# Performance work log

Hardware: AMD Instinct MI355X
Metric: run time of the kernel (lower is better)

## Reference

```python
import jax, jax.numpy as jnp
import numpy as np

B, N, NC, C = 8, 16384, 64, 256

def setup_inputs() -> dict:
    key = jax.random.key(0)
    k1, k2, k3, k4, k5, k6 = jax.random.split(key, 6)
    s = 1.0 / np.sqrt(C)
    return {
        "point_features": jax.random.normal(k1, (B, N, C), dtype=jnp.float32),
        "centroid_features": jax.random.normal(k2, (B, NC, C), dtype=jnp.float32),
        "W_p": jax.random.uniform(k3, (C, C), jnp.float32, -s, s),   # point_transform weight (in,out)
        "b_p": jax.random.uniform(k4, (C,), jnp.float32, -s, s),
        "W_c": jax.random.uniform(k5, (C, C), jnp.float32, -s, s),   # centroid_transform weight (in,out)
        "b_c": jax.random.uniform(k6, (C,), jnp.float32, -s, s),
    }

def reference(point_features, centroid_features, W_p, b_p, W_c, b_c):
    # Linear projections
    p_proj = jnp.einsum('bnc,cd->bnd', point_features, W_p) + b_p      # (B,N,C)
    c_proj = jnp.einsum('bkc,cd->bkd', centroid_features, W_c) + b_c   # (B,NC,C)
    # Unscaled cross-attention scores and softmax over centroids
    scores = jnp.einsum('bnd,bkd->bnk', p_proj, c_proj)                # (B,N,NC)
    weights = jax.nn.softmax(scores, axis=-1)
    # Weighted sum of RAW centroid features (values not projected)
    weighted = jnp.einsum('bnk,bkc->bnc', weights, centroid_features)  # (B,N,C)
    return point_features + weighted
```

## Files before the change

kernel.cpp:

```cpp
#include <hip/hip_runtime.h>

#define B_  8
#define N_  16384
#define NC_ 64
#define C_  256

typedef __attribute__((ext_vector_type(8))) short bf16x8;
typedef __attribute__((ext_vector_type(4))) float f32x4;

#define WS_GT   0
#define WS_BLOB 262144
#define WS_S0   786432
#define WS_WFB  788480
#define WS_H    789504
#define WS_BB   790528

__device__ __forceinline__ unsigned rne_bf16(float f) {
    unsigned u = __float_as_uint(f);
    return (u + 0x7fffu + ((u >> 16) & 1u)) >> 16;
}
__device__ __forceinline__ float bf2f(short s) {
    return __uint_as_float(((unsigned)(unsigned short)s) << 16);
}
__device__ __forceinline__ f32x4 mfma16(bf16x8 a, bf16x8 b, f32x4 c) {
    return __builtin_amdgcn_mfma_f32_16x16x32_bf16(a, b, c, 0, 0, 0);
}

__global__ __launch_bounds__(256) void k_p1(const float* __restrict__ Wp,
        const float* __restrict__ Wc, const float* __restrict__ bc,
        const float* __restrict__ bp, float* __restrict__ ws) {
    __shared__ float WpL[256];
    __shared__ float bpL[256];
    __shared__ float red[4];
    int c = blockIdx.x, t = threadIdx.x;
    WpL[t] = Wp[(size_t)c*C_ + t];
    bpL[t] = bp[t];
    float bcv = bc[t];
    __syncthreads();

    const float* wcr = Wc + (size_t)t*C_;
    float acc = 0.f;
    #pragma unroll 8
    for (int d = 0; d < C_; d += 4) {
        f32x4 wv = *(const f32x4*)(wcr + d);
        f32x4 wp = *(const f32x4*)(WpL + d);
        acc += wv[0]*wp[0] + wv[1]*wp[1] + wv[2]*wp[2] + wv[3]*wp[3];
    }
    ws[WS_GT/4 + c*C_ + t] = acc;

    float hp = bcv * WpL[t];
    #pragma unroll
    for (int m = 32; m; m >>= 1) hp += __shfl_xor(hp, m);
    if ((t & 63) == 0) red[t >> 6] = hp;
    __syncthreads();
    if (t == 0) ws[WS_H/4 + c] = red[0] + red[1] + red[2] + red[3];

    if (c == 0) {
        float aw = 0.f;
        #pragma unroll 8
        for (int d = 0; d < C_; d += 4) {
            f32x4 wv = *(const f32x4*)(wcr + d);
            f32x4 b4 = *(const f32x4*)(bpL + d);
            aw += wv[0]*b4[0] + wv[1]*b4[1] + wv[2]*b4[2] + wv[3]*b4[3];
        }
        ws[WS_WFB/4 + t] = aw;
        float pb = bcv * bpL[t];
        #pragma unroll
        for (int m = 32; m; m >>= 1) pb += __shfl_xor(pb, m);
        __syncthreads();
        if ((t & 63) == 0) red[t >> 6] = pb;
        __syncthreads();
        if (t == 0) ws[WS_BB/4] = red[0] + red[1] + red[2] + red[3];
    }
}

__global__ __launch_bounds__(256) void k_p2(const float* __restrict__ Cf,
        float* __restrict__ ws) {
    __shared__ float CfL[8][256];
    __shared__ float wfbL[256];
    int b = blockIdx.x >> 3, kg = blockIdx.x & 7;
    int t = threadIdx.x;
    const float* cfb = Cf + ((size_t)b*NC_ + kg*8)*C_;
    #pragma unroll
    for (int kk = 0; kk < 8; ++kk) CfL[kk][t] = cfb[kk*C_ + t];
    wfbL[t] = ws[WS_WFB/4 + t];
    float hv = ws[WS_H/4 + t];
    float bb = ws[WS_BB/4];
    __syncthreads();

    char* vtB  = (char*)ws + WS_BLOB + (size_t)b*65536;
    char* cftB = vtB + 32768;

    {
        int nf  = ((t >> 5) << 1) | ((t >> 2) & 1);
        int rho = ((t >> 3) & 3) * 4 + (t & 3);
        unsigned base = (unsigned)(nf*2048 + rho*128);
        #pragma unroll
        for (int kk = 0; kk < 8; ++kk) {
            *(unsigned short*)(cftB + base + (kg*8 + kk)*2) =
                (unsigned short)rne_bf16(CfL[kk][t]);
        }
    }

    float acc[8];
    #pragma unroll
    for (int kk = 0; kk < 8; ++kk) acc[kk] = hv;
    const float* gtr = ws + WS_GT/4 + (size_t)t*C_;
    #pragma unroll 4
    for (int e = 0; e < C_; e += 4) {
        f32x4 g4 = *(const f32x4*)(gtr + e);
        #pragma unroll
        for (int kk = 0; kk < 8; ++kk) {
            f32x4 c4 = *(const f32x4*)(&CfL[kk][e]);
            acc[kk] += g4[0]*c4[0] + g4[1]*c4[1] + g4[2]*c4[2] + g4[3]*c4[3];
        }
    }
    #pragma unroll
    for (int kk = 0; kk < 8; ++kk) {
        int row = kg*8 + kk;
        *(unsigned short*)(vtB + row*512 + t*2) = (unsigned short)rne_bf16(acc[kk]);
    }

    int w = t >> 6, l = t & 63;
    #pragma unroll
    for (int kk = 2*w; kk < 2*w + 2; ++kk) {
        float s = 0.f;
        #pragma unroll
        for (int j = 0; j < 4; ++j) s += CfL[kk][l + 64*j] * wfbL[l + 64*j];
        #pragma unroll
        for (int m = 32; m; m >>= 1) s += __shfl_xor(s, m);
        if (l == 0) ws[WS_S0/4 + b*NC_ + kg*8 + kk] = s + bb;
    }
}

__global__ __launch_bounds__(256, 4) void k_main(const float* __restrict__ P,
        const char* __restrict__ blob, const float* __restrict__ s0g,
        float* __restrict__ out) {
    __shared__ __align__(16) char wbAll[8192];

    int b    = blockIdx.x >> 8;
    int tile = blockIdx.x & 255;
    int tid = threadIdx.x;
    int w   = tid >> 6;
    int l   = tid & 63;
    int l15 = l & 15;
    int g   = l >> 4;

    const char* blobV = blob + (size_t)b*65536;
    const char* blobC = blobV + 32768;

    int prow = tile*64 + w*16 + l15;
    const float* Prow = P + ((size_t)b*N_ + prow)*C_;

    f32x4 sacc[4];
    #pragma unroll
    for (int mf = 0; mf < 4; ++mf)
        sacc[mf] = *(const f32x4*)(s0g + b*NC_ + mf*16 + g*4);

    bf16x8 phi[8], plo[8];
    f32x4 pA0 = *(const f32x4*)(Prow + g*8);
    f32x4 pA1 = *(const f32x4*)(Prow + g*8 + 4);
    f32x4 pB0 = *(const f32x4*)(Prow + g*8 + 32);
    f32x4 pB1 = *(const f32x4*)(Prow + g*8 + 36);

    #pragma unroll
    for (int kk = 0; kk < 8; ++kk) {
        bf16x8 vh0 = *(const bf16x8*)(blobV + (0*16 + l15)*512 + kk*64 + g*16);
        bf16x8 vh1 = *(const bf16x8*)(blobV + (1*16 + l15)*512 + kk*64 + g*16);
        bf16x8 vh2 = *(const bf16x8*)(blobV + (2*16 + l15)*512 + kk*64 + g*16);
        bf16x8 vh3 = *(const bf16x8*)(blobV + (3*16 + l15)*512 + kk*64 + g*16);
        #pragma unroll
        for (int h = 0; h < 2; ++h) {
            f32x4 src = h ? pA1 : pA0;
            #pragma unroll
            for (int j = 0; j < 4; ++j) {
                float f  = src[j];
                unsigned hb = rne_bf16(f);
                float hf = __uint_as_float(hb << 16);
                unsigned lb = rne_bf16(f - hf);
                phi[kk][h*4 + j] = (short)hb;
                plo[kk][h*4 + j] = (short)lb;
            }
        }
        pA0 = pB0; pA1 = pB1;
        if (kk < 6) {
            pB0 = *(const f32x4*)(Prow + g*8 + (kk+2)*32);
            pB1 = *(const f32x4*)(Prow + g*8 + (kk+2)*32 + 4);
        }
        sacc[0] = mfma16(vh0, phi[kk], sacc[0]);
        sacc[1] = mfma16(vh1, phi[kk], sacc[1]);
        sacc[2] = mfma16(vh2, phi[kk], sacc[2]);
        sacc[3] = mfma16(vh3, phi[kk], sacc[3]);
        sacc[0] = mfma16(vh0, plo[kk], sacc[0]);
        sacc[1] = mfma16(vh1, plo[kk], sacc[1]);
        sacc[2] = mfma16(vh2, plo[kk], sacc[2]);
        sacc[3] = mfma16(vh3, plo[kk], sacc[3]);
    }

    float mx = -3.0e38f;
    #pragma unroll
    for (int mf = 0; mf < 4; ++mf)
        #pragma unroll
        for (int r = 0; r < 4; ++r) mx = fmaxf(mx, sacc[mf][r]);
    mx = fmaxf(mx, __shfl_xor(mx, 16));
    mx = fmaxf(mx, __shfl_xor(mx, 32));
    float sum = 0.f;
    #pragma unroll
    for (int mf = 0; mf < 4; ++mf)
        #pragma unroll
        for (int r = 0; r < 4; ++r) {
            float e = __expf(sacc[mf][r] - mx);
            sacc[mf][r] = e; sum += e;
        }
    sum += __shfl_xor(sum, 16);
    sum += __shfl_xor(sum, 32);
    float inv = 1.0f / sum;

    char* wb = wbAll + w*2048;
    #pragma unroll
    for (int mf = 0; mf < 4; ++mf) {
        unsigned w01 = rne_bf16(sacc[mf][0]*inv) | (rne_bf16(sacc[mf][1]*inv) << 16);
        unsigned w23 = rne_bf16(sacc[mf][2]*inv) | (rne_bf16(sacc[mf][3]*inv) << 16);
        unsigned off = ((unsigned)(l15*128 + mf*32 + g*8)) ^ ((unsigned)(l15 & 7) << 4);
        uint2 v; v.x = w01; v.y = w23;
        *(uint2*)(wb + off) = v;
    }
    unsigned woff0 = ((unsigned)(l15*128 +  0 + g*16)) ^ ((unsigned)(l15 & 7) << 4);
    unsigned woff1 = ((unsigned)(l15*128 + 64 + g*16)) ^ ((unsigned)(l15 & 7) << 4);
    bf16x8 wf0 = *(const bf16x8*)(wb + woff0);
    bf16x8 wf1 = *(const bf16x8*)(wb + woff1);

    size_t rowbase = ((size_t)b*N_ + prow) * C_;
    #pragma unroll
    for (int nf = 0; nf < 16; ++nf) {
        const char* cbase = blobC + nf*2048 + l15*128 + g*16;
        bf16x8 cf0 = *(const bf16x8*)(cbase);
        bf16x8 cf1 = *(const bf16x8*)(cbase + 64);
        f32x4 o = {0.f, 0.f, 0.f, 0.f};
        o = mfma16(cf0, wf0, o);
        o = mfma16(cf1, wf1, o);
        int kf = nf >> 1, e0 = (nf & 1) * 4;
        f32x4 res;
        #pragma unroll
        for (int r = 0; r < 4; ++r)
            res[r] = bf2f(phi[kf][e0 + r]) + bf2f(plo[kf][e0 + r]) + o[r];
        *(f32x4*)(out + rowbase + (nf >> 1)*32 + (nf & 1)*4 + g*8) = res;
    }
}

extern "C" void kernel_launch(void* const* d_in, const int* in_sizes, int n_in,
                              void* d_out, int out_size, void* d_ws, size_t ws_size,
                              hipStream_t stream) {
    const float* P  = (const float*)d_in[0];
    const float* Cf = (const float*)d_in[1];
    const float* Wp = (const float*)d_in[2];
    const float* bp = (const float*)d_in[3];
    const float* Wc = (const float*)d_in[4];
    const float* bc = (const float*)d_in[5];
    float* out = (float*)d_out;
    float* ws  = (float*)d_ws;

    k_p1<<<256, 256, 0, stream>>>(Wp, Wc, bc, bp, ws);
    k_p2<<<64, 256, 0, stream>>>(Cf, ws);
    k_main<<<B_*(N_/64), 256, 0, stream>>>(P, (const char*)d_ws + WS_BLOB,
                                           ws + WS_S0/4, out);
}
```

Measured before the change: 354.7 us.

## Reload exact point features for residual and use natural centroid layout in output pass

The main kernel now issues all sixteen point-feature vector loads up front instead of a two-deep rolling prefetch. It drops the per-element bf16 hi/lo arrays kept alive across the softmax. The residual add now rereads the fp32 point features from global memory (likely L2-resident), using a simple contiguous column layout per output fragment. The centroid-value blob is written in a plain row-major transposed layout to match. This lowers register pressure and makes the residual exact, at the cost of a second read of the point rows and non-contiguous 16-byte output stores.

```diff
diff --git a/kernel.cpp b/kernel.cpp
--- a/kernel.cpp
+++ b/kernel.cpp
@@ -18,9 +18,6 @@
 __device__ __forceinline__ unsigned rne_bf16(float f) {
     unsigned u = __float_as_uint(f);
     return (u + 0x7fffu + ((u >> 16) & 1u)) >> 16;
-}
-__device__ __forceinline__ float bf2f(short s) {
-    return __uint_as_float(((unsigned)(unsigned short)s) << 16);
 }
 __device__ __forceinline__ f32x4 mfma16(bf16x8 a, bf16x8 b, f32x4 c) {
     return __builtin_amdgcn_mfma_f32_16x16x32_bf16(a, b, c, 0, 0, 0);
@@ -91,15 +88,10 @@
     char* vtB  = (char*)ws + WS_BLOB + (size_t)b*65536;
     char* cftB = vtB + 32768;
 
-    {
-        int nf  = ((t >> 5) << 1) | ((t >> 2) & 1);
-        int rho = ((t >> 3) & 3) * 4 + (t & 3);
-        unsigned base = (unsigned)(nf*2048 + rho*128);
-        #pragma unroll
-        for (int kk = 0; kk < 8; ++kk) {
-            *(unsigned short*)(cftB + base + (kg*8 + kk)*2) =
-                (unsigned short)rne_bf16(CfL[kk][t]);
-        }
+    #pragma unroll
+    for (int kk = 0; kk < 8; ++kk) {
+        *(unsigned short*)(cftB + t*128 + (kg*8 + kk)*2) =
+            (unsigned short)rne_bf16(CfL[kk][t]);
     }
 
     float acc[8];
@@ -150,18 +142,19 @@
     const char* blobC = blobV + 32768;
 
     int prow = tile*64 + w*16 + l15;
-    const float* Prow = P + ((size_t)b*N_ + prow)*C_;
-
+    size_t rowbase = ((size_t)b*N_ + prow) * C_;
+    const float* Prow = P + rowbase + g*8;
+
+    f32x4 pf[16];
+    #pragma unroll
+    for (int kk = 0; kk < 8; ++kk) {
+        pf[2*kk]   = *(const f32x4*)(Prow + kk*32);
+        pf[2*kk+1] = *(const f32x4*)(Prow + kk*32 + 4);
+    }
     f32x4 sacc[4];
     #pragma unroll
     for (int mf = 0; mf < 4; ++mf)
         sacc[mf] = *(const f32x4*)(s0g + b*NC_ + mf*16 + g*4);
-
-    bf16x8 phi[8], plo[8];
-    f32x4 pA0 = *(const f32x4*)(Prow + g*8);
-    f32x4 pA1 = *(const f32x4*)(Prow + g*8 + 4);
-    f32x4 pB0 = *(const f32x4*)(Prow + g*8 + 32);
-    f32x4 pB1 = *(const f32x4*)(Prow + g*8 + 36);
 
     #pragma unroll
     for (int kk = 0; kk < 8; ++kk) {
@@ -169,32 +162,28 @@
         bf16x8 vh1 = *(const bf16x8*)(blobV + (1*16 + l15)*512 + kk*64 + g*16);
         bf16x8 vh2 = *(const bf16x8*)(blobV + (2*16 + l15)*512 + kk*64 + g*16);
         bf16x8 vh3 = *(const bf16x8*)(blobV + (3*16 + l15)*512 + kk*64 + g*16);
+        bf16x8 phi, plo;
         #pragma unroll
         for (int h = 0; h < 2; ++h) {
-            f32x4 src = h ? pA1 : pA0;
+            f32x4 src = h ? pf[2*kk+1] : pf[2*kk];
             #pragma unroll
             for (int j = 0; j < 4; ++j) {
                 float f  = src[j];
                 unsigned hb = rne_bf16(f);
                 float hf = __uint_as_float(hb << 16);
                 unsigned lb = rne_bf16(f - hf);
-                phi[kk][h*4 + j] = (short)hb;
-                plo[kk][h*4 + j] = (short)lb;
+                phi[h*4 + j] = (short)hb;
+                plo[h*4 + j] = (short)lb;
             }
         }
-        pA0 = pB0; pA1 = pB1;
-        if (kk < 6) {
-            pB0 = *(const f32x4*)(Prow + g*8 + (kk+2)*32);
-            pB1 = *(const f32x4*)(Prow + g*8 + (kk+2)*32 + 4);
-        }
-        sacc[0] = mfma16(vh0, phi[kk], sacc[0]);
-        sacc[1] = mfma16(vh1, phi[kk], sacc[1]);
-        sacc[2] = mfma16(vh2, phi[kk], sacc[2]);
-        sacc[3] = mfma16(vh3, phi[kk], sacc[3]);
-        sacc[0] = mfma16(vh0, plo[kk], sacc[0]);
-        sacc[1] = mfma16(vh1, plo[kk], sacc[1]);
-        sacc[2] = mfma16(vh2, plo[kk], sacc[2]);
-        sacc[3] = mfma16(vh3, plo[kk], sacc[3]);
+        sacc[0] = mfma16(vh0, phi, sacc[0]);
+        sacc[1] = mfma16(vh1, phi, sacc[1]);
+        sacc[2] = mfma16(vh2, phi, sacc[2]);
+        sacc[3] = mfma16(vh3, phi, sacc[3]);
+        sacc[0] = mfma16(vh0, plo, sacc[0]);
+        sacc[1] = mfma16(vh1, plo, sacc[1]);
+        sacc[2] = mfma16(vh2, plo, sacc[2]);
+        sacc[3] = mfma16(vh3, plo, sacc[3]);
     }
 
     float mx = -3.0e38f;
@@ -230,21 +219,17 @@
     bf16x8 wf0 = *(const bf16x8*)(wb + woff0);
     bf16x8 wf1 = *(const bf16x8*)(wb + woff1);
 
-    size_t rowbase = ((size_t)b*N_ + prow) * C_;
     #pragma unroll
     for (int nf = 0; nf < 16; ++nf) {
-        const char* cbase = blobC + nf*2048 + l15*128 + g*16;
+        const char* cbase = blobC + (nf*16 + l15)*128 + g*16;
         bf16x8 cf0 = *(const bf16x8*)(cbase);
         bf16x8 cf1 = *(const bf16x8*)(cbase + 64);
+        f32x4 pr = *(const f32x4*)(P + rowbase + nf*16 + g*4);
         f32x4 o = {0.f, 0.f, 0.f, 0.f};
         o = mfma16(cf0, wf0, o);
         o = mfma16(cf1, wf1, o);
-        int kf = nf >> 1, e0 = (nf & 1) * 4;
-        f32x4 res;
-        #pragma unroll
-        for (int r = 0; r < 4; ++r)
-            res[r] = bf2f(phi[kf][e0 + r]) + bf2f(plo[kf][e0 + r]) + o[r];
-        *(f32x4*)(out + rowbase + (nf >> 1)*32 + (nf & 1)*4 + g*8) = res;
+        f32x4 res = {pr[0]+o[0], pr[1]+o[1], pr[2]+o[2], pr[3]+o[3]};
+        *(f32x4*)(out + rowbase + nf*16 + g*4) = res;
     }
 }
 
```

New measurement: 321.3 us. 1.1x faster.
